# Kernel tuning notes

Measured on AMD Instinct MI355X. Metric: run time of the kernel, lower is better.

## Reference

```python
import jax, jax.numpy as jnp
import numpy as np
from itertools import combinations

N_QUBITS = 8
PAIRS = list(combinations(range(N_QUBITS), 2))  # 28 qubit pairs -> 28 features/node

# qubit 0 = first tensor factor (most significant bit of the basis index)
CNOT01 = jnp.array([[1,0,0,0],[0,1,0,0],[0,0,0,1],[0,0,1,0]], dtype=jnp.complex64)  # control q0, target q1
CNOT10 = jnp.array([[1,0,0,0],[0,0,0,1],[0,0,1,0],[0,1,0,0]], dtype=jnp.complex64)  # control q1, target q0
I2 = jnp.eye(2, dtype=jnp.complex64)
HZ = jnp.array([1.0, -1.0, 1.0, -1.0], dtype=jnp.complex64)  # diag(I kron Z)


def _rx(t):
    c = jnp.cos(t / 2).astype(jnp.complex64)
    s = jnp.sin(t / 2).astype(jnp.complex64)
    return jnp.stack([jnp.stack([c, -1j * s]), jnp.stack([-1j * s, c])])


def _ry(t):
    c = jnp.cos(t / 2).astype(jnp.complex64)
    s = jnp.sin(t / 2).astype(jnp.complex64)
    return jnp.stack([jnp.stack([c, -s]), jnp.stack([s, c])])


def _rz(t):
    e = jnp.exp(-0.5j * t.astype(jnp.complex64))
    z = jnp.zeros((), jnp.complex64)
    return jnp.stack([jnp.stack([e, z]), jnp.stack([z, jnp.conj(e)])])


def _pair_unitary(p):  # p: [6] params for one qubit pair
    A = _rz(p[5]) @ _ry(p[4]) @ _rx(p[3]) @ _rz(p[2]) @ _ry(p[1]) @ _rx(p[0])
    return CNOT01 @ (CNOT10 @ jnp.kron(A, I2))  # [4,4]


def _quantum_features(x, qweight):
    """Batched version of the per-node amplitude encoding + 28 two-qubit circuits."""
    N = x.shape[0]
    psi = (x / jnp.linalg.norm(x, axis=1, keepdims=True)).astype(jnp.complex64)  # [N,256]
    psi8 = psi.reshape((N,) + (2,) * N_QUBITS)
    Us = jax.vmap(_pair_unitary)(qweight.reshape(len(PAIRS), 6))  # [28,4,4]
    cols = []
    for p, (a, b) in enumerate(PAIRS):
        perm = (0, 1 + a, 1 + b) + tuple(1 + q for q in range(N_QUBITS) if q not in (a, b))
        v = jnp.transpose(psi8, perm).reshape(N, 4, 2 ** (N_QUBITS - 2))  # [N,4,64]
        rho = jnp.einsum('nim,njm->nij', v, jnp.conj(v))  # reduced 2-qubit DM [N,4,4]
        U = Us[p]
        # <I kron Z> after U rho U^dagger, mapped to [0,1]
        e = jnp.einsum('a,ab,nbc,ac->n', HZ, U, rho, jnp.conj(U))
        cols.append((jnp.real(e) + 1.0) * 0.5)
    return jnp.stack(cols, axis=1).astype(jnp.float32)  # [N,28]


def reference(x, edge_index, qweight, W1, b1, W2, b2):
    N = x.shape[0]
    x_deal = _quantum_features(x, qweight)  # [N,28]
    # gcn_norm with added self loops, edge_weight = 1
    loop = jnp.arange(N)
    src = jnp.concatenate([edge_index[0], loop])
    dst = jnp.concatenate([edge_index[1], loop])
    w = jnp.ones(src.shape[0], dtype=jnp.float32)
    deg = jax.ops.segment_sum(w, dst, num_segments=N)
    dinv = jax.lax.rsqrt(jnp.maximum(deg, 1e-12))
    norm = dinv[src] * w * dinv[dst]
    out = jax.ops.segment_sum(norm[:, None] * x_deal[src], dst, num_segments=N)  # [N,28]
    out = jax.nn.relu(out)
    g = (out.T @ out).reshape(1, 28 * 28)  # [1,784]
    h = jax.nn.relu(g @ W1.T + b1)
    return jax.nn.sigmoid(h @ W2.T + b2)  # [1,1]


def setup_inputs() -> dict:
    N, F, E = 50000, 256, 1600000
    key = jax.random.key(0)
    ks = jax.random.split(key, 6)
    x = jax.random.normal(ks[0], (N, F), dtype=jnp.float32)
    edge_index = jax.random.randint(ks[1], (2, E), 0, N, dtype=jnp.int64)
    qweight = jax.random.uniform(ks[2], (168,), dtype=jnp.float32) * (2.0 * np.pi)
    W1 = jax.random.normal(ks[3], (128, 784), dtype=jnp.float32) * 0.03
    b1 = jnp.zeros((128,), dtype=jnp.float32)
    W2 = jax.random.normal(ks[4], (1, 128), dtype=jnp.float32) * 0.08
    b2 = jnp.zeros((1,), dtype=jnp.float32)
    return {"x": x, "edge_index": edge_index, "qweight": qweight,
            "W1": W1, "b1": b1, "W2": W2, "b2": b2}
```

## Files before the change

kernel.cpp:

```cpp
#include <hip/hip_runtime.h>
#include <hip/hip_fp16.h>
#include <math.h>

#define N_NODES 50000
#define N_EDGES 1600000
#define BSHIFT 6
#define NB_BUCKETS 782
#define PART_CHUNK 8192
#define NCHUNK 196
#define CAP 3072
#define ZSTRIDE 32

template<int CTRL>
__device__ inline float dpp_mov(float x){
    return __int_as_float(__builtin_amdgcn_update_dpp(0, __float_as_int(x), CTRL, 0xf, 0xf, false));
}
__device__ inline float wave_sum_dpp(float x){
    x += dpp_mov<0x111>(x);
    x += dpp_mov<0x112>(x);
    x += dpp_mov<0x114>(x);
    x += dpp_mov<0x118>(x);
    x += dpp_mov<0x142>(x);
    x += dpp_mov<0x143>(x);
    return x;
}
__device__ inline float lane63(float x){
    return __int_as_float(__builtin_amdgcn_readlane(__float_as_int(x), 63));
}
#define DPP_XOR1 0xB1
#define DPP_XOR2 0x4E

struct C2 { float x, y; };
__device__ inline C2 mkc(float x, float y){ C2 r; r.x=x; r.y=y; return r; }
__device__ inline C2 cmul(C2 a, C2 b){ return mkc(a.x*b.x - a.y*b.y, a.x*b.y + a.y*b.x); }
__device__ inline C2 cadd(C2 a, C2 b){ return mkc(a.x+b.x, a.y+b.y); }

__global__ __launch_bounds__(256) void k_init(const float* __restrict__ qw,
        const void* __restrict__ ei, float4* __restrict__ cmat,
        int* __restrict__ flag, int* __restrict__ bucketFill, float* __restrict__ G){
    int t = threadIdx.x;
    for (int i = t; i < NB_BUCKETS; i += 256) bucketFill[i] = 0;
    for (int i = t; i < 784; i += 256) G[i] = 0.f;
    if (t == 255){
        const long long* e64 = (const long long*)ei;
        int ok = 1;
        for (int i = 0; i < 64; i++){
            long long v = e64[i];
            if (v < 0 || v >= N_NODES) ok = 0;
        }
        flag[0] = ok;
    }
    if (t < 28){
        int p = t;
        int a = 0; { int rem = p, q = 0; while (rem >= 7 - q){ rem -= 7 - q; q++; } a = q; }
        C2 M00 = mkc(1,0), M01 = mkc(0,0), M10 = mkc(0,0), M11 = mkc(1,0);
        for (int k = 0; k < 6; k++){
            float th = 0.5f * qw[p*6 + k];
            float s, c; sincosf(th, &s, &c);
            C2 R00, R01, R10, R11;
            int type = k % 3;
            if (type == 0){
                R00 = mkc(c,0); R01 = mkc(0,-s); R10 = mkc(0,-s); R11 = mkc(c,0);
            } else if (type == 1){
                R00 = mkc(c,0); R01 = mkc(-s,0); R10 = mkc(s,0); R11 = mkc(c,0);
            } else {
                R00 = mkc(c,-s); R01 = mkc(0,0); R10 = mkc(0,0); R11 = mkc(c,s);
            }
            C2 N00 = cadd(cmul(R00,M00), cmul(R01,M10));
            C2 N01 = cadd(cmul(R00,M01), cmul(R01,M11));
            C2 N10 = cadd(cmul(R10,M00), cmul(R11,M10));
            C2 N11 = cadd(cmul(R10,M01), cmul(R11,M11));
            M00=N00; M01=N01; M10=N10; M11=N11;
        }
        float B00  = (M00.x*M00.x + M00.y*M00.y) - (M10.x*M10.x + M10.y*M10.y);
        float B11  = (M01.x*M01.x + M01.y*M01.y) - (M11.x*M11.x + M11.y*M11.y);
        float B01r = (M00.x*M01.x + M00.y*M01.y) - (M10.x*M11.x + M10.y*M11.y);
        cmat[p] = make_float4(0.5f + 0.5f*B11, 0.5f*(B00 - B11), B01r, (float)a);
    }
}

__device__ inline int get_edge(const void* ei, int is64, long long idx){
    if (is64) return (int)((const long long*)ei)[idx];
    return ((const int*)ei)[idx];
}

__global__ __launch_bounds__(1024) void k_part(const void* __restrict__ ei,
        const int* __restrict__ flag, int* __restrict__ bucketFill,
        unsigned* __restrict__ pairs){
    __shared__ int hist[NB_BUCKETS];
    __shared__ int cntb[NB_BUCKETS];
    __shared__ int cursor[NB_BUCKETS];
    __shared__ int copyBase[NB_BUCKETS];
    __shared__ unsigned sorted[PART_CHUNK];
    int tid = threadIdx.x, c = blockIdx.x;
    long long base = (long long)c * PART_CHUNK;
    int cnt = (int)((N_EDGES - base < PART_CHUNK) ? (N_EDGES - base) : PART_CHUNK);
    int is64 = flag[0];
    unsigned ds[8], sr[8];
    #pragma unroll
    for (int k = 0; k < 8; k++){
        int i = tid + 1024*k;
        if (i < cnt){
            ds[k] = (unsigned)get_edge(ei, is64, (long long)N_EDGES + base + i);
            sr[k] = (unsigned)get_edge(ei, is64, base + i);
        } else ds[k] = 0xffffffffu;
    }
    if (tid < NB_BUCKETS) hist[tid] = 0;
    __syncthreads();
    #pragma unroll
    for (int k = 0; k < 8; k++)
        if (ds[k] != 0xffffffffu) atomicAdd(&hist[ds[k] >> BSHIFT], 1);
    __syncthreads();
    if (tid < NB_BUCKETS) cntb[tid] = hist[tid];
    __syncthreads();
    for (int ofs = 1; ofs < NB_BUCKETS; ofs <<= 1){
        int v = 0; bool a = tid < NB_BUCKETS;
        if (a) v = hist[tid] + (tid >= ofs ? hist[tid - ofs] : 0);
        __syncthreads();
        if (a) hist[tid] = v;
        __syncthreads();
    }
    if (tid < NB_BUCKETS){
        int cb = cntb[tid];
        int ls = hist[tid] - cb;
        int gbase = tid*CAP + atomicAdd(&bucketFill[tid], cb);
        copyBase[tid] = gbase - ls;
        cursor[tid] = ls;
    }
    __syncthreads();
    #pragma unroll
    for (int k = 0; k < 8; k++){
        if (ds[k] != 0xffffffffu){
            int pos = atomicAdd(&cursor[ds[k] >> BSHIFT], 1);
            sorted[pos] = (ds[k] << 16) | sr[k];
        }
    }
    __syncthreads();
    for (int i = tid; i < cnt; i += 1024){
        unsigned v = sorted[i];
        int b = (int)(v >> 22);
        pairs[copyBase[b] + i] = v;
    }
}

__global__ __launch_bounds__(256) void k_sort(const unsigned* __restrict__ pairs,
        const int* __restrict__ bucketFill, unsigned short* __restrict__ csr,
        int* __restrict__ nodeOff, float* __restrict__ dinv){
    __shared__ unsigned short sorted[CAP];
    __shared__ int hist[64];
    __shared__ int cursor[64];
    int b = blockIdx.x, t = threadIdx.x;
    int s0 = b*CAP;
    int cnt = bucketFill[b];
    if (cnt > CAP) cnt = CAP;
    if (t < 64) hist[t] = 0;
    __syncthreads();
    for (int i = t; i < cnt; i += 256){
        unsigned v = pairs[s0 + i];
        atomicAdd(&hist[(v >> 16) & 63], 1);
    }
    __syncthreads();
    int mycnt = (t < 64) ? hist[t] : 0;
    for (int ofs = 1; ofs < 64; ofs <<= 1){
        int nv = 0;
        if (t < 64) nv = hist[t] + (t >= ofs ? hist[t - ofs] : 0);
        __syncthreads();
        if (t < 64) hist[t] = nv;
        __syncthreads();
    }
    if (t < 64){
        cursor[t] = hist[t] - mycnt;
        int n = b*64 + t;
        if (n < N_NODES){
            nodeOff[n] = s0 + hist[t] - mycnt;
            dinv[n] = rsqrtf((float)(mycnt + 1));
        }
    }
    __syncthreads();
    for (int i = t; i < cnt; i += 256){
        unsigned v = pairs[s0 + i];
        int d = (v >> 16) & 63;
        int pos = atomicAdd(&cursor[d], 1);
        sorted[pos] = (unsigned short)(v & 0xffffu);
    }
    __syncthreads();
    for (int i = t; i < cnt; i += 256) csr[s0 + i] = sorted[i];
}

__global__ __launch_bounds__(256) void k_feat(const float* __restrict__ x,
        const float* __restrict__ dinv, const float4* __restrict__ cmat,
        __half* __restrict__ z){
    int wave = threadIdx.x >> 6;
    int lane = threadIdx.x & 63;
    int n = blockIdx.x*4 + wave;
    const float4 v = ((const float4*)(x + (size_t)n*256))[lane];
    float persq = v.x*v.x + v.y*v.y + v.z*v.z + v.w*v.w;

    float red[15];
    red[0] = persq;
    red[1] = v.x*v.x + v.y*v.y;
    red[2] = v.x*v.z + v.y*v.w;
    {
        float px = dpp_mov<DPP_XOR1>(v.x), py = dpp_mov<DPP_XOR1>(v.y);
        float pz = dpp_mov<DPP_XOR1>(v.z), pw = dpp_mov<DPP_XOR1>(v.w);
        red[3] = v.x*px + v.y*py + v.z*pz + v.w*pw;
        red[9] = (lane & 1) ? 0.f : persq;
    }
    {
        float px = dpp_mov<DPP_XOR2>(v.x), py = dpp_mov<DPP_XOR2>(v.y);
        float pz = dpp_mov<DPP_XOR2>(v.z), pw = dpp_mov<DPP_XOR2>(v.w);
        red[4] = v.x*px + v.y*py + v.z*pz + v.w*pw;
        red[10] = (lane & 2) ? 0.f : persq;
    }
    #pragma unroll
    for (int j = 2; j < 6; j++){
        float px = __shfl_xor(v.x, 1 << j), py = __shfl_xor(v.y, 1 << j);
        float pz = __shfl_xor(v.z, 1 << j), pw = __shfl_xor(v.w, 1 << j);
        red[3 + j] = v.x*px + v.y*py + v.z*pz + v.w*pw;
        red[9 + j] = ((lane >> j) & 1) ? 0.0f : persq;
    }
    float S[15];
    #pragma unroll
    for (int k = 0; k < 15; k++) S[k] = lane63(wave_sum_dpp(red[k]));

    if (lane < 28){
        float4 cm = cmat[lane];
        int ap = (int)cm.w;
        float S0a = (ap==6) ? S[1] :
                    (ap==0 ? S[14] : ap==1 ? S[13] : ap==2 ? S[12] :
                     ap==3 ? S[11] : ap==4 ? S[10] : S[9]);
        float Xa  = (ap==6) ? S[2] :
                    0.5f*(ap==0 ? S[8] : ap==1 ? S[7] : ap==2 ? S[6] :
                          ap==3 ? S[5] : ap==4 ? S[4] : S[3]);
        float feat = cm.x + (cm.y*S0a + cm.z*Xa) / S[0];
        z[(size_t)n*ZSTRIDE + lane] = __float2half(dinv[n] * feat);
    } else if (lane < 32){
        z[(size_t)n*ZSTRIDE + lane] = __float2half(0.f);
    }
}

__device__ inline void acc_pack(unsigned u, float& a, float& b){
    float2 f = __half22float2(__builtin_bit_cast(__half2, u));
    a += f.x; b += f.y;
}
__device__ inline void acc_row(const uint4* rp, float* acc ){
    uint4 w0 = rp[0], w1 = rp[1], w2 = rp[2], w3 = rp[3];
    acc_pack(w0.x, acc[0],  acc[1]);  acc_pack(w0.y, acc[2],  acc[3]);
    acc_pack(w0.z, acc[4],  acc[5]);  acc_pack(w0.w, acc[6],  acc[7]);
    acc_pack(w1.x, acc[8],  acc[9]);  acc_pack(w1.y, acc[10], acc[11]);
    acc_pack(w1.z, acc[12], acc[13]); acc_pack(w1.w, acc[14], acc[15]);
    acc_pack(w2.x, acc[16], acc[17]); acc_pack(w2.y, acc[18], acc[19]);
    acc_pack(w2.z, acc[20], acc[21]); acc_pack(w2.w, acc[22], acc[23]);
    acc_pack(w3.x, acc[24], acc[25]); acc_pack(w3.y, acc[26], acc[27]);
    acc_pack(w3.z, acc[28], acc[29]); acc_pack(w3.w, acc[30], acc[31]);
}

__global__ __launch_bounds__(256) void k_gather(const unsigned short* __restrict__ csr,
        const int* __restrict__ nodeOff, const int* __restrict__ bucketFill,
        const __half* __restrict__ z, const float* __restrict__ dinv,
        float* __restrict__ out){
    int g = blockIdx.x*256 + threadIdx.x;
    int n = g >> 2, sub = g & 3;
    if (n >= N_NODES) return;
    int b = n >> 6, d = n & 63;
    int beg = nodeOff[n];
    int end = (d == 63 || n == N_NODES - 1) ? b*CAP + min(bucketFill[b], CAP)
                                            : nodeOff[n + 1];
    float acc[32];
    #pragma unroll
    for (int k = 0; k < 32; k++) acc[k] = 0.f;
    for (int i = beg + sub; i < end; i += 4){
        int src = csr[i];
        acc_row((const uint4*)(z + (size_t)src*ZSTRIDE), acc);
    }
    if (sub == 3) acc_row((const uint4*)(z + (size_t)n*ZSTRIDE), acc);
    #pragma unroll
    for (int k = 0; k < 32; k++){
        acc[k] += dpp_mov<DPP_XOR1>(acc[k]);
        acc[k] += dpp_mov<DPP_XOR2>(acc[k]);
    }
    if (sub == 0){
        float dv = dinv[n];
        float4* o = (float4*)(out + (size_t)n*28);
        #pragma unroll
        for (int q = 0; q < 7; q++)
            o[q] = make_float4(fmaxf(acc[4*q+0]*dv, 0.f), fmaxf(acc[4*q+1]*dv, 0.f),
                               fmaxf(acc[4*q+2]*dv, 0.f), fmaxf(acc[4*q+3]*dv, 0.f));
    }
}

__global__ __launch_bounds__(256) void k_gram(const float* __restrict__ out, float* __restrict__ G){
    __shared__ float buf[64*28];
    int tid = threadIdx.x;
    bool val = tid < 196;
    int ti = val ? tid / 14 : 0, tj = val ? tid % 14 : 0;
    int i0 = 2*ti, j0 = 2*tj;
    float c00 = 0.f, c01 = 0.f, c10 = 0.f, c11 = 0.f;
    int nchunks = (N_NODES + 63) / 64;
    for (int ch = blockIdx.x; ch < nchunks; ch += gridDim.x){
        int base = ch * 64;
        int total = (N_NODES - base < 64 ? N_NODES - base : 64) * 28;
        __syncthreads();
        for (int t = tid; t < 64*28; t += 256)
            buf[t] = (t < total) ? out[(size_t)base*28 + t] : 0.f;
        __syncthreads();
        for (int nn = 0; nn < 64; nn++){
            const float* r = buf + nn*28;
            float a0 = r[i0], a1 = r[i0+1], b0 = r[j0], b1 = r[j0+1];
            c00 += a0*b0; c01 += a0*b1; c10 += a1*b0; c11 += a1*b1;
        }
    }
    if (val){
        atomicAdd(&G[(i0  )*28 + j0  ], c00);
        atomicAdd(&G[(i0  )*28 + j0+1], c01);
        atomicAdd(&G[(i0+1)*28 + j0  ], c10);
        atomicAdd(&G[(i0+1)*28 + j0+1], c11);
    }
}

__global__ __launch_bounds__(256) void k_mlp(const float* __restrict__ G,
        const float* __restrict__ W1, const float* __restrict__ b1,
        const float* __restrict__ W2, const float* __restrict__ b2,
        float* __restrict__ outp){
    __shared__ float part[256];
    __shared__ float h[128];
    int t = threadIdx.x;
    int j = t & 127, halfsel = t >> 7;
    const float* w = W1 + (size_t)j*784 + halfsel*392;
    const float* g = G + halfsel*392;
    float s = 0.f;
    for (int i = 0; i < 392; i++) s += g[i] * w[i];
    part[t] = s;
    __syncthreads();
    if (t < 128) h[t] = fmaxf(part[t] + part[t+128] + b1[t], 0.f) * W2[t];
    __syncthreads();
    for (int ofs = 64; ofs > 0; ofs >>= 1){
        if (t < ofs) h[t] += h[t + ofs];
        __syncthreads();
    }
    if (t == 0) outp[0] = 1.f / (1.f + expf(-(h[0] + b2[0])));
}

extern "C" void kernel_launch(void* const* d_in, const int* in_sizes, int n_in,
                              void* d_out, int out_size, void* d_ws, size_t ws_size,
                              hipStream_t stream){
    const float* x  = (const float*)d_in[0];
    const void*  ei = d_in[1];
    const float* qw = (const float*)d_in[2];
    const float* W1 = (const float*)d_in[3];
    const float* b1 = (const float*)d_in[4];
    const float* W2 = (const float*)d_in[5];
    const float* b2 = (const float*)d_in[6];
    float* outp = (float*)d_out;

    char* base = (char*)d_ws;
    __half*         z     = (__half*)base;         base += (size_t)N_NODES*ZSTRIDE*2;
    float*          ob    = (float*)base;          base += (size_t)N_NODES*28*4;
    unsigned*       pairs = (unsigned*)base;       base += (size_t)NB_BUCKETS*CAP*4;
    unsigned short* csr   = (unsigned short*)base; base += (size_t)NB_BUCKETS*CAP*2;
    int*            nodeOff = (int*)base;          base += (size_t)N_NODES*4;
    float*          dinv  = (float*)base;          base += (size_t)N_NODES*4;
    float4*         cmat  = (float4*)base;         base += 448;
    float*          G     = (float*)base;          base += 4096;
    int*            bucketFill = (int*)base;       base += 4096;
    int*            flag  = (int*)base;            base += 16;

    k_init<<<1, 256, 0, stream>>>(qw, ei, cmat, flag, bucketFill, G);
    k_part<<<NCHUNK, 1024, 0, stream>>>(ei, flag, bucketFill, pairs);
    k_sort<<<NB_BUCKETS, 256, 0, stream>>>(pairs, bucketFill, csr, nodeOff, dinv);
    k_feat<<<N_NODES/4, 256, 0, stream>>>(x, dinv, cmat, z);
    k_gather<<<(N_NODES*4 + 255)/256, 256, 0, stream>>>(csr, nodeOff, bucketFill, z, dinv, ob);
    k_gram<<<196, 256, 0, stream>>>(ob, G);
    k_mlp<<<1, 256, 0, stream>>>(G, W1, b1, W2, b2, outp);
}
```

Before: 205.1 us.

## Fuse bucket sort, neighbor gather, and Gram accumulation into one per-bucket kernel

Node degrees are now counted with global atomics during partitioning, so k_feat computes dinv itself. The per-bucket counting sort, the neighbor gather and the Gram matrix partials are merged into a single k_bucket kernel that keeps the CSR and the aggregated rows in shared memory. This removes the csr/nodeOff/out round trips through global memory and two kernel launches. In exchange it adds 1.6M global atomics on deg, and there are 782 Gram atomic flushes instead of 196.

```diff
diff --git a/kernel.cpp b/kernel.cpp
--- a/kernel.cpp
+++ b/kernel.cpp
@@ -37,8 +37,11 @@
 
 __global__ __launch_bounds__(256) void k_init(const float* __restrict__ qw,
         const void* __restrict__ ei, float4* __restrict__ cmat,
-        int* __restrict__ flag, int* __restrict__ bucketFill, float* __restrict__ G){
+        int* __restrict__ flag, int* __restrict__ bucketFill, float* __restrict__ G,
+        int* __restrict__ deg){
     int t = threadIdx.x;
+    for (int i = blockIdx.x*256 + t; i < N_NODES; i += 64*256) deg[i] = 0;
+    if (blockIdx.x != 0) return;
     for (int i = t; i < NB_BUCKETS; i += 256) bucketFill[i] = 0;
     for (int i = t; i < 784; i += 256) G[i] = 0.f;
     if (t == 255){
@@ -86,7 +89,7 @@
 
 __global__ __launch_bounds__(1024) void k_part(const void* __restrict__ ei,
         const int* __restrict__ flag, int* __restrict__ bucketFill,
-        unsigned* __restrict__ pairs){
+        unsigned* __restrict__ pairs, int* __restrict__ deg){
     __shared__ int hist[NB_BUCKETS];
     __shared__ int cntb[NB_BUCKETS];
     __shared__ int cursor[NB_BUCKETS];
@@ -109,7 +112,10 @@
     __syncthreads();
     #pragma unroll
     for (int k = 0; k < 8; k++)
-        if (ds[k] != 0xffffffffu) atomicAdd(&hist[ds[k] >> BSHIFT], 1);
+        if (ds[k] != 0xffffffffu){
+            atomicAdd(&hist[ds[k] >> BSHIFT], 1);
+            atomicAdd(&deg[ds[k]], 1);
+        }
     __syncthreads();
     if (tid < NB_BUCKETS) cntb[tid] = hist[tid];
     __syncthreads();
@@ -143,53 +149,9 @@
     }
 }
 
-__global__ __launch_bounds__(256) void k_sort(const unsigned* __restrict__ pairs,
-        const int* __restrict__ bucketFill, unsigned short* __restrict__ csr,
-        int* __restrict__ nodeOff, float* __restrict__ dinv){
-    __shared__ unsigned short sorted[CAP];
-    __shared__ int hist[64];
-    __shared__ int cursor[64];
-    int b = blockIdx.x, t = threadIdx.x;
-    int s0 = b*CAP;
-    int cnt = bucketFill[b];
-    if (cnt > CAP) cnt = CAP;
-    if (t < 64) hist[t] = 0;
-    __syncthreads();
-    for (int i = t; i < cnt; i += 256){
-        unsigned v = pairs[s0 + i];
-        atomicAdd(&hist[(v >> 16) & 63], 1);
-    }
-    __syncthreads();
-    int mycnt = (t < 64) ? hist[t] : 0;
-    for (int ofs = 1; ofs < 64; ofs <<= 1){
-        int nv = 0;
-        if (t < 64) nv = hist[t] + (t >= ofs ? hist[t - ofs] : 0);
-        __syncthreads();
-        if (t < 64) hist[t] = nv;
-        __syncthreads();
-    }
-    if (t < 64){
-        cursor[t] = hist[t] - mycnt;
-        int n = b*64 + t;
-        if (n < N_NODES){
-            nodeOff[n] = s0 + hist[t] - mycnt;
-            dinv[n] = rsqrtf((float)(mycnt + 1));
-        }
-    }
-    __syncthreads();
-    for (int i = t; i < cnt; i += 256){
-        unsigned v = pairs[s0 + i];
-        int d = (v >> 16) & 63;
-        int pos = atomicAdd(&cursor[d], 1);
-        sorted[pos] = (unsigned short)(v & 0xffffu);
-    }
-    __syncthreads();
-    for (int i = t; i < cnt; i += 256) csr[s0 + i] = sorted[i];
-}
-
 __global__ __launch_bounds__(256) void k_feat(const float* __restrict__ x,
-        const float* __restrict__ dinv, const float4* __restrict__ cmat,
-        __half* __restrict__ z){
+        const int* __restrict__ deg, const float4* __restrict__ cmat,
+        __half* __restrict__ z, float* __restrict__ dinv){
     int wave = threadIdx.x >> 6;
     int lane = threadIdx.x & 63;
     int n = blockIdx.x*4 + wave;
@@ -223,6 +185,8 @@
     #pragma unroll
     for (int k = 0; k < 15; k++) S[k] = lane63(wave_sum_dpp(red[k]));
 
+    float dvn = rsqrtf((float)(deg[n] + 1));
+    if (lane == 0) dinv[n] = dvn;
     if (lane < 28){
         float4 cm = cmat[lane];
         int ap = (int)cm.w;
@@ -233,7 +197,7 @@
                     0.5f*(ap==0 ? S[8] : ap==1 ? S[7] : ap==2 ? S[6] :
                           ap==3 ? S[5] : ap==4 ? S[4] : S[3]);
         float feat = cm.x + (cm.y*S0a + cm.z*Xa) / S[0];
-        z[(size_t)n*ZSTRIDE + lane] = __float2half(dinv[n] * feat);
+        z[(size_t)n*ZSTRIDE + lane] = __float2half(dvn * feat);
     } else if (lane < 32){
         z[(size_t)n*ZSTRIDE + lane] = __float2half(0.f);
     }
@@ -255,62 +219,84 @@
     acc_pack(w3.z, acc[28], acc[29]); acc_pack(w3.w, acc[30], acc[31]);
 }
 
-__global__ __launch_bounds__(256) void k_gather(const unsigned short* __restrict__ csr,
-        const int* __restrict__ nodeOff, const int* __restrict__ bucketFill,
-        const __half* __restrict__ z, const float* __restrict__ dinv,
-        float* __restrict__ out){
-    int g = blockIdx.x*256 + threadIdx.x;
-    int n = g >> 2, sub = g & 3;
-    if (n >= N_NODES) return;
-    int b = n >> 6, d = n & 63;
-    int beg = nodeOff[n];
-    int end = (d == 63 || n == N_NODES - 1) ? b*CAP + min(bucketFill[b], CAP)
-                                            : nodeOff[n + 1];
+__global__ __launch_bounds__(256) void k_bucket(const unsigned* __restrict__ pairs,
+        const int* __restrict__ bucketFill, const __half* __restrict__ z,
+        const float* __restrict__ dinv, float* __restrict__ G){
+    __shared__ unsigned short sorted[CAP];
+    __shared__ int hist[64];
+    __shared__ int cursor[64];
+    __shared__ int begs[64];
+    __shared__ int cnts[64];
+    __shared__ float srow[64*28];
+    int b = blockIdx.x, t = threadIdx.x;
+    int s0 = b*CAP;
+    int cnt = bucketFill[b];
+    if (cnt > CAP) cnt = CAP;
+    if (t < 64) hist[t] = 0;
+    __syncthreads();
+    for (int i = t; i < cnt; i += 256){
+        unsigned v = pairs[s0 + i];
+        atomicAdd(&hist[(v >> 16) & 63], 1);
+    }
+    __syncthreads();
+    int mycnt = (t < 64) ? hist[t] : 0;
+    for (int ofs = 1; ofs < 64; ofs <<= 1){
+        int nv = 0;
+        if (t < 64) nv = hist[t] + (t >= ofs ? hist[t - ofs] : 0);
+        __syncthreads();
+        if (t < 64) hist[t] = nv;
+        __syncthreads();
+    }
+    if (t < 64){
+        cursor[t] = hist[t] - mycnt;
+        begs[t]   = hist[t] - mycnt;
+        cnts[t]   = mycnt;
+    }
+    __syncthreads();
+    for (int i = t; i < cnt; i += 256){
+        unsigned v = pairs[s0 + i];
+        int d = (v >> 16) & 63;
+        int pos = atomicAdd(&cursor[d], 1);
+        sorted[pos] = (unsigned short)(v & 0xffffu);
+    }
+    __syncthreads();
+
+    int d = t >> 2, sub = t & 3;
+    int n = b*64 + d;
+    bool valid = n < N_NODES;
     float acc[32];
     #pragma unroll
     for (int k = 0; k < 32; k++) acc[k] = 0.f;
-    for (int i = beg + sub; i < end; i += 4){
-        int src = csr[i];
-        acc_row((const uint4*)(z + (size_t)src*ZSTRIDE), acc);
-    }
-    if (sub == 3) acc_row((const uint4*)(z + (size_t)n*ZSTRIDE), acc);
+    if (valid){
+        int beg = begs[d], end = beg + cnts[d];
+        for (int i = beg + sub; i < end; i += 4){
+            int src = sorted[i];
+            acc_row((const uint4*)(z + (size_t)src*ZSTRIDE), acc);
+        }
+        if (sub == 3) acc_row((const uint4*)(z + (size_t)n*ZSTRIDE), acc);
+    }
     #pragma unroll
     for (int k = 0; k < 32; k++){
         acc[k] += dpp_mov<DPP_XOR1>(acc[k]);
         acc[k] += dpp_mov<DPP_XOR2>(acc[k]);
     }
     if (sub == 0){
-        float dv = dinv[n];
-        float4* o = (float4*)(out + (size_t)n*28);
+        float dv = valid ? dinv[n] : 0.f;
         #pragma unroll
-        for (int q = 0; q < 7; q++)
-            o[q] = make_float4(fmaxf(acc[4*q+0]*dv, 0.f), fmaxf(acc[4*q+1]*dv, 0.f),
-                               fmaxf(acc[4*q+2]*dv, 0.f), fmaxf(acc[4*q+3]*dv, 0.f));
-    }
-}
-
-__global__ __launch_bounds__(256) void k_gram(const float* __restrict__ out, float* __restrict__ G){
-    __shared__ float buf[64*28];
-    int tid = threadIdx.x;
-    bool val = tid < 196;
-    int ti = val ? tid / 14 : 0, tj = val ? tid % 14 : 0;
-    int i0 = 2*ti, j0 = 2*tj;
-    float c00 = 0.f, c01 = 0.f, c10 = 0.f, c11 = 0.f;
-    int nchunks = (N_NODES + 63) / 64;
-    for (int ch = blockIdx.x; ch < nchunks; ch += gridDim.x){
-        int base = ch * 64;
-        int total = (N_NODES - base < 64 ? N_NODES - base : 64) * 28;
-        __syncthreads();
-        for (int t = tid; t < 64*28; t += 256)
-            buf[t] = (t < total) ? out[(size_t)base*28 + t] : 0.f;
-        __syncthreads();
+        for (int k = 0; k < 28; k++)
+            srow[d*28 + k] = fmaxf(acc[k]*dv, 0.f);
+    }
+    __syncthreads();
+
+    if (t < 196){
+        int ti = t / 14, tj = t % 14;
+        int i0 = 2*ti, j0 = 2*tj;
+        float c00 = 0.f, c01 = 0.f, c10 = 0.f, c11 = 0.f;
         for (int nn = 0; nn < 64; nn++){
-            const float* r = buf + nn*28;
+            const float* r = srow + nn*28;
             float a0 = r[i0], a1 = r[i0+1], b0 = r[j0], b1 = r[j0+1];
             c00 += a0*b0; c01 += a0*b1; c10 += a1*b0; c11 += a1*b1;
         }
-    }
-    if (val){
         atomicAdd(&G[(i0  )*28 + j0  ], c00);
         atomicAdd(&G[(i0  )*28 + j0+1], c01);
         atomicAdd(&G[(i0+1)*28 + j0  ], c10);
@@ -355,21 +341,17 @@
 
     char* base = (char*)d_ws;
     __half*         z     = (__half*)base;         base += (size_t)N_NODES*ZSTRIDE*2;
-    float*          ob    = (float*)base;          base += (size_t)N_NODES*28*4;
     unsigned*       pairs = (unsigned*)base;       base += (size_t)NB_BUCKETS*CAP*4;
-    unsigned short* csr   = (unsigned short*)base; base += (size_t)NB_BUCKETS*CAP*2;
-    int*            nodeOff = (int*)base;          base += (size_t)N_NODES*4;
+    int*            deg   = (int*)base;            base += (size_t)N_NODES*4;
     float*          dinv  = (float*)base;          base += (size_t)N_NODES*4;
     float4*         cmat  = (float4*)base;         base += 448;
     float*          G     = (float*)base;          base += 4096;
     int*            bucketFill = (int*)base;       base += 4096;
     int*            flag  = (int*)base;            base += 16;
 
-    k_init<<<1, 256, 0, stream>>>(qw, ei, cmat, flag, bucketFill, G);
-    k_part<<<NCHUNK, 1024, 0, stream>>>(ei, flag, bucketFill, pairs);
-    k_sort<<<NB_BUCKETS, 256, 0, stream>>>(pairs, bucketFill, csr, nodeOff, dinv);
-    k_feat<<<N_NODES/4, 256, 0, stream>>>(x, dinv, cmat, z);
-    k_gather<<<(N_NODES*4 + 255)/256, 256, 0, stream>>>(csr, nodeOff, bucketFill, z, dinv, ob);
-    k_gram<<<196, 256, 0, stream>>>(ob, G);
+    k_init<<<64, 256, 0, stream>>>(qw, ei, cmat, flag, bucketFill, G, deg);
+    k_part<<<NCHUNK, 1024, 0, stream>>>(ei, flag, bucketFill, pairs, deg);
+    k_feat<<<N_NODES/4, 256, 0, stream>>>(x, deg, cmat, z, dinv);
+    k_bucket<<<NB_BUCKETS, 256, 0, stream>>>(pairs, bucketFill, z, dinv, G);
     k_mlp<<<1, 256, 0, stream>>>(G, W1, b1, W2, b2, outp);
 }
```

Measured after the change: 304.6 us. +48.6%, slower.

## Fuse Gram accumulation into gather kernel via shared-memory row tile

Applied to the files above, without the earlier changes.

The gather kernel now writes each block's 64 aggregated ReLU rows into shared memory and computes the partial 28x28 Gram product in place, atomically adding to G. This removes the separate Gram kernel, one launch, and the round trip of the N x 28 intermediate through global memory. In exchange, atomic traffic on G grows from 196 blocks to 782 blocks, and each gather block now carries an extra serial Gram phase.

```diff
diff --git a/kernel.cpp b/kernel.cpp
--- a/kernel.cpp
+++ b/kernel.cpp
@@ -258,59 +258,48 @@
 __global__ __launch_bounds__(256) void k_gather(const unsigned short* __restrict__ csr,
         const int* __restrict__ nodeOff, const int* __restrict__ bucketFill,
         const __half* __restrict__ z, const float* __restrict__ dinv,
-        float* __restrict__ out){
-    int g = blockIdx.x*256 + threadIdx.x;
-    int n = g >> 2, sub = g & 3;
-    if (n >= N_NODES) return;
-    int b = n >> 6, d = n & 63;
-    int beg = nodeOff[n];
-    int end = (d == 63 || n == N_NODES - 1) ? b*CAP + min(bucketFill[b], CAP)
-                                            : nodeOff[n + 1];
+        float* __restrict__ G){
+    __shared__ float srow[64*28];
+    int t = threadIdx.x;
+    int n = blockIdx.x*64 + (t >> 2), sub = t & 3;
+    bool valid = n < N_NODES;
     float acc[32];
     #pragma unroll
     for (int k = 0; k < 32; k++) acc[k] = 0.f;
-    for (int i = beg + sub; i < end; i += 4){
-        int src = csr[i];
-        acc_row((const uint4*)(z + (size_t)src*ZSTRIDE), acc);
-    }
-    if (sub == 3) acc_row((const uint4*)(z + (size_t)n*ZSTRIDE), acc);
+    if (valid){
+        int b = n >> 6, d = n & 63;
+        int beg = nodeOff[n];
+        int end = (d == 63 || n == N_NODES - 1) ? b*CAP + min(bucketFill[b], CAP)
+                                                : nodeOff[n + 1];
+        for (int i = beg + sub; i < end; i += 4){
+            int src = csr[i];
+            acc_row((const uint4*)(z + (size_t)src*ZSTRIDE), acc);
+        }
+        if (sub == 3) acc_row((const uint4*)(z + (size_t)n*ZSTRIDE), acc);
+    }
     #pragma unroll
     for (int k = 0; k < 32; k++){
         acc[k] += dpp_mov<DPP_XOR1>(acc[k]);
         acc[k] += dpp_mov<DPP_XOR2>(acc[k]);
     }
     if (sub == 0){
-        float dv = dinv[n];
-        float4* o = (float4*)(out + (size_t)n*28);
+        float dv = valid ? dinv[n] : 0.f;
+        int d = (t >> 2);
         #pragma unroll
-        for (int q = 0; q < 7; q++)
-            o[q] = make_float4(fmaxf(acc[4*q+0]*dv, 0.f), fmaxf(acc[4*q+1]*dv, 0.f),
-                               fmaxf(acc[4*q+2]*dv, 0.f), fmaxf(acc[4*q+3]*dv, 0.f));
-    }
-}
-
-__global__ __launch_bounds__(256) void k_gram(const float* __restrict__ out, float* __restrict__ G){
-    __shared__ float buf[64*28];
-    int tid = threadIdx.x;
-    bool val = tid < 196;
-    int ti = val ? tid / 14 : 0, tj = val ? tid % 14 : 0;
-    int i0 = 2*ti, j0 = 2*tj;
-    float c00 = 0.f, c01 = 0.f, c10 = 0.f, c11 = 0.f;
-    int nchunks = (N_NODES + 63) / 64;
-    for (int ch = blockIdx.x; ch < nchunks; ch += gridDim.x){
-        int base = ch * 64;
-        int total = (N_NODES - base < 64 ? N_NODES - base : 64) * 28;
-        __syncthreads();
-        for (int t = tid; t < 64*28; t += 256)
-            buf[t] = (t < total) ? out[(size_t)base*28 + t] : 0.f;
-        __syncthreads();
+        for (int k = 0; k < 28; k++)
+            srow[d*28 + k] = fmaxf(acc[k]*dv, 0.f);
+    }
+    __syncthreads();
+
+    if (t < 196){
+        int ti = t / 14, tj = t % 14;
+        int i0 = 2*ti, j0 = 2*tj;
+        float c00 = 0.f, c01 = 0.f, c10 = 0.f, c11 = 0.f;
         for (int nn = 0; nn < 64; nn++){
-            const float* r = buf + nn*28;
+            const float* r = srow + nn*28;
             float a0 = r[i0], a1 = r[i0+1], b0 = r[j0], b1 = r[j0+1];
             c00 += a0*b0; c01 += a0*b1; c10 += a1*b0; c11 += a1*b1;
         }
-    }
-    if (val){
         atomicAdd(&G[(i0  )*28 + j0  ], c00);
         atomicAdd(&G[(i0  )*28 + j0+1], c01);
         atomicAdd(&G[(i0+1)*28 + j0  ], c10);
@@ -355,7 +344,6 @@
 
     char* base = (char*)d_ws;
     __half*         z     = (__half*)base;         base += (size_t)N_NODES*ZSTRIDE*2;
-    float*          ob    = (float*)base;          base += (size_t)N_NODES*28*4;
     unsigned*       pairs = (unsigned*)base;       base += (size_t)NB_BUCKETS*CAP*4;
     unsigned short* csr   = (unsigned short*)base; base += (size_t)NB_BUCKETS*CAP*2;
     int*            nodeOff = (int*)base;          base += (size_t)N_NODES*4;
@@ -369,7 +357,6 @@
     k_part<<<NCHUNK, 1024, 0, stream>>>(ei, flag, bucketFill, pairs);
     k_sort<<<NB_BUCKETS, 256, 0, stream>>>(pairs, bucketFill, csr, nodeOff, dinv);
     k_feat<<<N_NODES/4, 256, 0, stream>>>(x, dinv, cmat, z);
-    k_gather<<<(N_NODES*4 + 255)/256, 256, 0, stream>>>(csr, nodeOff, bucketFill, z, dinv, ob);
-    k_gram<<<196, 256, 0, stream>>>(ob, G);
+    k_gather<<<NB_BUCKETS, 256, 0, stream>>>(csr, nodeOff, bucketFill, z, dinv, G);
     k_mlp<<<1, 256, 0, stream>>>(G, W1, b1, W2, b2, outp);
 }
```

New measurement: 254.2 us. +24.0%, slower.
